# Performance work log

Measured on AMD Instinct MI355X. Metric: run time of the kernel, lower is better.

The kernel has to match this reference:

```python
import jax, jax.numpy as jnp
import numpy as np

E = 8      # n_rm_states
D = 256    # flattened input dim
H = 64     # hidden width (hard-coded in module)
A = 18     # n_actions
B = 65536  # batch


def setup_inputs() -> dict:
    key = jax.random.key(0)
    ks = jax.random.split(key, 16)
    s = lambda k, shape, fan_in: jax.random.normal(k, shape, jnp.float32) * (1.0 / np.sqrt(fan_in))
    inp = {
        "state": jax.random.normal(ks[0], (B, D), jnp.float32),
        "rm_state": jax.random.randint(ks[1], (B,), 0, E),
        # stacked per-expert params: layer i weight [E, in, out], bias [E, out]
        "W1": s(ks[2], (E, D, H), D), "b1": jnp.zeros((E, H), jnp.float32),
        "W2": s(ks[3], (E, H, H), H), "b2": jnp.zeros((E, H), jnp.float32),
        "W3": s(ks[4], (E, H, H), H), "b3": jnp.zeros((E, H), jnp.float32),
        "W4": s(ks[5], (E, H, H), H), "b4": jnp.zeros((E, H), jnp.float32),
        "W5": s(ks[6], (E, H, H), H), "b5": jnp.zeros((E, H), jnp.float32),
        "W6": s(ks[7], (E, H, A), H), "b6": jnp.zeros((E, A), jnp.float32),
    }
    return inp


def reference(state, rm_state, W1, b1, W2, b2, W3, b3, W4, b4, W5, b5, W6, b6):
    x = state.reshape(state.shape[0], -1)              # [B, D]
    # Run all E expert MLPs densely over the batch, then select per-row expert.
    h = jax.nn.relu(jnp.einsum('bd,edh->ebh', x, W1) + b1[:, None, :])   # [E, B, H]
    h = jax.nn.relu(jnp.einsum('ebh,ehk->ebk', h, W2) + b2[:, None, :])
    h = jax.nn.relu(jnp.einsum('ebh,ehk->ebk', h, W3) + b3[:, None, :])
    h = jax.nn.relu(jnp.einsum('ebh,ehk->ebk', h, W4) + b4[:, None, :])
    h = jax.nn.relu(jnp.einsum('ebh,ehk->ebk', h, W5) + b5[:, None, :])
    out_all = jnp.einsum('ebh,eha->eba', h, W6) + b6[:, None, :]          # [E, B, A]
    # scatter-back: actions[b] = expert[rm_state[b]](x[b])
    actions = out_all[rm_state, jnp.arange(x.shape[0])]                    # [B, A]
    return actions
```

## Files before the change

kernel.cpp:

```cpp
#include <hip/hip_runtime.h>
#include <hip/hip_bf16.h>


#define NE   8
#define DIM  256
#define HID  64
#define NA   18

typedef __attribute__((ext_vector_type(8))) short short8;
typedef __attribute__((ext_vector_type(4))) float f32x4;
#define MFMA __builtin_amdgcn_mfma_f32_16x16x32_bf16

__device__ __forceinline__ unsigned short f2bf(float f) {
    unsigned u = __builtin_bit_cast(unsigned, f);
    u += 0x7fff + ((u >> 16) & 1);
    return (unsigned short)(u >> 16);
}
__device__ __forceinline__ float bf2f(unsigned short h) {
    unsigned u = ((unsigned)h) << 16;
    return __builtin_bit_cast(float, u);
}
__device__ __forceinline__ void split8v(const float* xs, short8& hi, short8& lo) {
    float back[8];
    #pragma unroll
    for (int p = 0; p < 4; ++p) {
        __hip_bfloat162 h2 = __float22bfloat162_rn(make_float2(xs[2*p], xs[2*p+1]));
        hi[2*p]   = (short)__builtin_bit_cast(unsigned short, h2.x);
        hi[2*p+1] = (short)__builtin_bit_cast(unsigned short, h2.y);
        float2 b2 = __bfloat1622float2(h2);
        back[2*p] = b2.x; back[2*p+1] = b2.y;
    }
    #pragma unroll
    for (int p = 0; p < 4; ++p) {
        __hip_bfloat162 l2 = __float22bfloat162_rn(
            make_float2(xs[2*p] - back[2*p], xs[2*p+1] - back[2*p+1]));
        lo[2*p]   = (short)__builtin_bit_cast(unsigned short, l2.x);
        lo[2*p+1] = (short)__builtin_bit_cast(unsigned short, l2.y);
    }
}

__global__ __launch_bounds__(256) void prep_histo(
    const float* __restrict__ W1, const float* __restrict__ W2,
    const float* __restrict__ W3, const float* __restrict__ W4,
    const float* __restrict__ W5, const float* __restrict__ W6,
    short* __restrict__ W1H, short* __restrict__ W1L,
    short* __restrict__ W2H, short* __restrict__ W2L,
    short* __restrict__ W3H, short* __restrict__ W3L,
    short* __restrict__ W4H, short* __restrict__ W4L,
    short* __restrict__ W5H, short* __restrict__ W5L,
    short* __restrict__ W6H, short* __restrict__ W6L,
    const int* __restrict__ rm, int* __restrict__ hist) {
    const int bid = blockIdx.x;
    if (bid >= 136) {
        __shared__ int wch[4][NE];
        const int blk = bid - 136;
        const int t = threadIdx.x, w = t >> 6, l = t & 63;
        const int e = rm[blk * 256 + t];
        #pragma unroll
        for (int q = 0; q < NE; ++q) {
            unsigned long long m = __ballot(e == q);
            if (l == 0) wch[w][q] = __popcll(m);
        }
        __syncthreads();
        if (t < NE) hist[blk * NE + t] = wch[0][t] + wch[1][t] + wch[2][t] + wch[3][t];
        return;
    }
    const int u = bid * 256 + threadIdx.x;
    const float* src; int sstride, dbase, n, npad;
    short *H, *L;
    if (u < 16384) {
        int e = u >> 11, r = u & 2047;
        int ks = r >> 8, nt = (r >> 6) & 3, l = r & 63;
        int k0 = ks * 32 + ((l >> 4) << 3); n = (nt << 4) + (l & 15);
        src = W1 + ((size_t)(e * DIM + k0)) * HID + n;
        sstride = HID; npad = HID;
        H = W1H; L = W1L; dbase = e * 16384 + ((ks * 4 + nt) * 64 + l) * 8;
    } else if (u < 32768) {
        int u2 = u - 16384;
        int layer = u2 >> 12, local = u2 & 4095;
        int e = local >> 9, r = local & 511;
        int ks = r >> 8, nt = (r >> 6) & 3, l = r & 63;
        int k0 = ks * 32 + ((l >> 4) << 3); n = (nt << 4) + (l & 15);
        const float* W = (layer == 0) ? W2 : (layer == 1) ? W3 : (layer == 2) ? W4 : W5;
        src = W + ((size_t)(e * HID + k0)) * HID + n;
        sstride = HID; npad = HID;
        H = (layer == 0) ? W2H : (layer == 1) ? W3H : (layer == 2) ? W4H : W5H;
        L = (layer == 0) ? W2L : (layer == 1) ? W3L : (layer == 2) ? W4L : W5L;
        dbase = e * 4096 + ((ks * 4 + nt) * 64 + l) * 8;
    } else {
        int u3 = u - 32768;
        int e = u3 >> 8, r = u3 & 255;
        int ks = r >> 7, nt = (r >> 6) & 1, l = r & 63;
        int k0 = ks * 32 + ((l >> 4) << 3); n = (nt << 4) + (l & 15);
        src = W6 + ((size_t)(e * HID + k0)) * NA + n;
        sstride = NA; npad = NA;
        H = W6H; L = W6L; dbase = e * 2048 + ((ks * 2 + nt) * 64 + l) * 8;
    }
    short8 hs, ls;
    #pragma unroll
    for (int j = 0; j < 8; ++j) {
        float v = (n < npad) ? src[j * sstride] : 0.0f;
        unsigned short h = f2bf(v);
        hs[j] = (short)h;
        ls[j] = (short)f2bf(v - bf2f(h));
    }
    *(short8*)(H + dbase) = hs;
    *(short8*)(L + dbase) = ls;
}

__global__ __launch_bounds__(512) void scan_scatter(const int* __restrict__ rm,
                                                    const int* __restrict__ hist,
                                                    int* __restrict__ perm,
                                                    int* __restrict__ meta) {
    __shared__ int sbuf[NE][256];
    __shared__ int wc[8][NE];
    __shared__ int wb2[4][NE];
    __shared__ int baseE[NE];
    const int t = threadIdx.x, w = t >> 6, l = t & 63;
    const int myblk = blockIdx.x;

    {
        int v0 = hist[(l * 4 + 0) * NE + w];
        int v1 = hist[(l * 4 + 1) * NE + w];
        int v2 = hist[(l * 4 + 2) * NE + w];
        int v3 = hist[(l * 4 + 3) * NE + w];
        v1 += v0; v2 += v1; v3 += v2;
        int s = v3;
        #pragma unroll
        for (int off = 1; off < 64; off <<= 1) {
            int u = __shfl_up(s, off);
            if (l >= off) s += u;
        }
        const int ex = s - v3;
        sbuf[w][l * 4 + 0] = ex + v0;
        sbuf[w][l * 4 + 1] = ex + v1;
        sbuf[w][l * 4 + 2] = ex + v2;
        sbuf[w][l * 4 + 3] = ex + v3;
    }
    __syncthreads();
    if (t < NE) {
        int es = 0;
        for (int q = 0; q < t; ++q) es += sbuf[q][255];
        baseE[t] = es + (myblk ? sbuf[t][myblk - 1] : 0);
    }
    if (myblk == 0 && t == 0) {
        int es = 0, ts = 0;
        meta[8] = 0; meta[17] = 0;
        for (int e = 0; e < NE; ++e) {
            int c = sbuf[e][255];
            meta[e] = c;
            es += c; meta[8 + e + 1] = es;
            ts += (c + 31) >> 5; meta[17 + e + 1] = ts;
        }
    }
    const int i = myblk * 256 + t;
    const int e_row = (t < 256) ? rm[i] : -1;
    const unsigned long long ltm = (1ull << l) - 1ull;
    int rank = 0;
    #pragma unroll
    for (int q = 0; q < NE; ++q) {
        unsigned long long m = __ballot(e_row == q);
        if (e_row == q) rank = __popcll(m & ltm);
        if (l == 0) wc[w][q] = __popcll(m);
    }
    __syncthreads();
    if (t < 32) {
        int ww = t >> 3, q = t & 7;
        int b = baseE[q];
        for (int p = 0; p < ww; ++p) b += wc[p][q];
        wb2[ww][q] = b;
    }
    __syncthreads();
    if (t < 256) perm[wb2[w][e_row] + rank] = i;
}

__device__ __forceinline__ void read_split(const float* pa, const float* pb, int off,
                                           short8& hi, short8& lo) {
    float4 a0 = *(const float4*)(pa + off);
    float4 a1 = *(const float4*)(pa + off + 4);
    float4 b0 = *(const float4*)(pb + off);
    float4 b1 = *(const float4*)(pb + off + 4);
    float xs[8] = {fmaxf(a0.x + b0.x, 0.0f), fmaxf(a0.y + b0.y, 0.0f),
                   fmaxf(a0.z + b0.z, 0.0f), fmaxf(a0.w + b0.w, 0.0f),
                   fmaxf(a1.x + b1.x, 0.0f), fmaxf(a1.y + b1.y, 0.0f),
                   fmaxf(a1.z + b1.z, 0.0f), fmaxf(a1.w + b1.w, 0.0f)};
    split8v(xs, hi, lo);
}

template <int NT>
__device__ __forceinline__ void mfma_slice(const short* __restrict__ WH,
                                           const short* __restrict__ WL,
                                           int l, int kh,
                                           const short8& ahi, const short8& alo,
                                           f32x4* acc) {
    #pragma unroll
    for (int nt = 0; nt < NT; ++nt) {
        short8 bh = *(const short8*)(WH + (kh * NT + nt) * 512 + l * 8);
        short8 bl = *(const short8*)(WL + (kh * NT + nt) * 512 + l * 8);
        acc[nt] = MFMA(ahi, bh, acc[nt], 0, 0, 0);
        acc[nt] = MFMA(alo, bh, acc[nt], 0, 0, 0);
        acc[nt] = MFMA(ahi, bl, acc[nt], 0, 0, 0);
    }
}

template <int NT>
__device__ __forceinline__ void write_partial(float* pw, int l,
                                              const float* __restrict__ bias,
                                              const f32x4* acc) {
    const int lg = l >> 4, lr = l & 15;
    #pragma unroll
    for (int nt = 0; nt < NT; ++nt) {
        float bv = bias ? bias[nt * 16 + lr] : 0.0f;
        #pragma unroll
        for (int r = 0; r < 4; ++r)
            pw[(lg * 4 + r) * 68 + nt * 16 + lr] = acc[nt][r] + bv;
    }
}

__global__ __launch_bounds__(256, 8) void mlp_mfma(
    const float* __restrict__ x, const int* __restrict__ perm,
    const int* __restrict__ meta,
    const short* __restrict__ W1H, const short* __restrict__ W1L,
    const short* __restrict__ W2H, const short* __restrict__ W2L,
    const short* __restrict__ W3H, const short* __restrict__ W3L,
    const short* __restrict__ W4H, const short* __restrict__ W4L,
    const short* __restrict__ W5H, const short* __restrict__ W5L,
    const short* __restrict__ W6H, const short* __restrict__ W6L,
    const float* __restrict__ b1, const float* __restrict__ b2,
    const float* __restrict__ b3, const float* __restrict__ b4,
    const float* __restrict__ b5, const float* __restrict__ b6,
    float* __restrict__ out) {
    __shared__ __align__(16) float hbuf[2][2][16][68];
    const int blk = blockIdx.x;
    if (blk >= meta[17 + NE]) return;
    int e = 0;
    #pragma unroll 1
    while (blk >= meta[17 + e + 1]) ++e;
    const int lt = blk - meta[17 + e];
    const int cnt = meta[e];
    const int pbase = meta[8 + e];
    const int t = threadIdx.x, w = t >> 6, l = t & 63;
    const int m = w >> 1, kh = w & 1;
    const int lg = l >> 4, lr = l & 15;
    const int li = lt * 32 + m * 16 + lr;
    const int row = perm[pbase + min(li, cnt - 1)];

    float* pw = &hbuf[kh][m][0][0];
    const float* pa = &hbuf[0][m][0][0];
    const float* pb = &hbuf[1][m][0][0];
    const int roff = lr * 68 + kh * 32 + lg * 8;
    const f32x4 zero = {0.0f, 0.0f, 0.0f, 0.0f};

    {
        f32x4 a0[4] = {zero, zero, zero, zero};
        f32x4 a1[4] = {zero, zero, zero, zero};
        const float* xr = x + (size_t)row * DIM + kh * 128 + lg * 8;
        const short* WHp = W1H + (size_t)e * 16384;
        const short* WLp = W1L + (size_t)e * 16384;
        #pragma unroll
        for (int ks = 0; ks < 4; ++ks) {
            float4 u0 = *(const float4*)(xr + ks * 32);
            float4 u1 = *(const float4*)(xr + ks * 32 + 4);
            float xs[8] = {u0.x, u0.y, u0.z, u0.w, u1.x, u1.y, u1.z, u1.w};
            short8 ahi, alo; split8v(xs, ahi, alo);
            const int ksg = kh * 4 + ks;
            #pragma unroll
            for (int nt = 0; nt < 4; ++nt) {
                short8 bh = *(const short8*)(WHp + (ksg * 4 + nt) * 512 + l * 8);
                short8 bl = *(const short8*)(WLp + (ksg * 4 + nt) * 512 + l * 8);
                a0[nt] = MFMA(ahi, bh, a0[nt], 0, 0, 0);
                a1[nt] = MFMA(alo, bh, a1[nt], 0, 0, 0);
                a1[nt] = MFMA(ahi, bl, a1[nt], 0, 0, 0);
            }
        }
        f32x4 acc[4];
        #pragma unroll
        for (int nt = 0; nt < 4; ++nt) acc[nt] = a0[nt] + a1[nt];
        write_partial<4>(pw, l, (kh == 0) ? b1 + e * HID : nullptr, acc);
    }
    __syncthreads();

    #define HIDDEN(WH_, WL_, bias_)                                          \
    {                                                                        \
        short8 ahi, alo;                                                     \
        read_split(pa, pb, roff, ahi, alo);                                  \
        __syncthreads();                    \
        f32x4 acc[4] = {zero, zero, zero, zero};                             \
        mfma_slice<4>(WH_ + e * 4096, WL_ + e * 4096, l, kh, ahi, alo, acc); \
        write_partial<4>(pw, l, (kh == 0) ? bias_ + e * HID : nullptr, acc); \
        __syncthreads();                   \
    }
    HIDDEN(W2H, W2L, b2)
    HIDDEN(W3H, W3L, b3)
    HIDDEN(W4H, W4L, b4)
    HIDDEN(W5H, W5L, b5)
    #undef HIDDEN

    {
        short8 ahi, alo;
        read_split(pa, pb, roff, ahi, alo);
        __syncthreads();
        f32x4 acc[2] = {zero, zero};
        mfma_slice<2>(W6H + e * 2048, W6L + e * 2048, l, kh, ahi, alo, acc);
        write_partial<2>(pw, l, nullptr, acc);
        __syncthreads();
    }
    const float* b6p = b6 + e * NA;
    #pragma unroll
    for (int idx = t; idx < 2 * 16 * NA; idx += 256) {
        const int m2 = idx / (16 * NA);
        const int rr = (idx % (16 * NA)) / NA;
        const int c  = idx % NA;
        const int gr = lt * 32 + m2 * 16 + rr;
        if (gr < cnt) {
            const int rowid = perm[pbase + gr];
            out[(size_t)rowid * NA + c] =
                hbuf[0][m2][rr][c] + hbuf[1][m2][rr][c] + b6p[c];
        }
    }
}

extern "C" void kernel_launch(void* const* d_in, const int* in_sizes, int n_in,
                              void* d_out, int out_size, void* d_ws, size_t ws_size,
                              hipStream_t stream) {
    const float* x  = (const float*)d_in[0];
    const int*   rm = (const int*)d_in[1];
    const float* W1 = (const float*)d_in[2];   const float* b1 = (const float*)d_in[3];
    const float* W2 = (const float*)d_in[4];   const float* b2 = (const float*)d_in[5];
    const float* W3 = (const float*)d_in[6];   const float* b3 = (const float*)d_in[7];
    const float* W4 = (const float*)d_in[8];   const float* b4 = (const float*)d_in[9];
    const float* W5 = (const float*)d_in[10];  const float* b5 = (const float*)d_in[11];
    const float* W6 = (const float*)d_in[12];  const float* b6 = (const float*)d_in[13];
    float* out = (float*)d_out;

    const int B = in_sizes[1];
    const int nblk = B / 256;

    int* hist = (int*)d_ws;
    int* meta = hist + nblk * NE;
    int* perm = meta + 32;
    short* W1H = (short*)(perm + B);
    short* W1L = W1H + 131072;
    short* W2H = W1L + 131072;  short* W2L = W2H + 32768;
    short* W3H = W2L + 32768;   short* W3L = W3H + 32768;
    short* W4H = W3L + 32768;   short* W4L = W4H + 32768;
    short* W5H = W4L + 32768;   short* W5L = W5H + 32768;
    short* W6H = W5L + 32768;   short* W6L = W6H + 16384;

    prep_histo<<<136 + nblk, 256, 0, stream>>>(W1, W2, W3, W4, W5, W6,
                                               W1H, W1L, W2H, W2L, W3H, W3L,
                                               W4H, W4L, W5H, W5L, W6H, W6L,
                                               rm, hist);
    scan_scatter<<<nblk, 512, 0, stream>>>(rm, hist, perm, meta);
    mlp_mfma<<<B / 32 + NE, 256, 0, stream>>>(x, perm, meta,
                                              W1H, W1L, W2H, W2L, W3H, W3L,
                                              W4H, W4L, W5H, W5L, W6H, W6L,
                                              b1, b2, b3, b4, b5, b6, out);
}
```

Measured before the change: 153.1 us.

## Switch MLP to 32x32x16 MFMA with 128-row tiles and weight prefetch

Replaces the 16x16x32 bf16 MFMA path with 32x32x16 MFMAs, repacking all weight fragments in the prep kernel to match the new operand layout. Each block now processes 128 rows with 512 threads instead of 32 rows with 256, so there are fewer tiles per expert, and the scan metadata is updated to count 128-row tiles. Weight fragments for the next layer are loaded into registers before the current layer's MFMAs to hide load latency. The trade-offs are higher register pressure, fewer resident blocks, and more padded work for experts whose row count is not a multiple of 128.

New measurement: 162.7 us. 6.2% more time.

```diff
diff --git a/kernel.cpp b/kernel.cpp
--- a/kernel.cpp
+++ b/kernel.cpp
@@ -7,9 +7,9 @@
 #define HID  64
 #define NA   18
 
-typedef __attribute__((ext_vector_type(8))) short short8;
-typedef __attribute__((ext_vector_type(4))) float f32x4;
-#define MFMA __builtin_amdgcn_mfma_f32_16x16x32_bf16
+typedef __attribute__((ext_vector_type(8)))  short short8;
+typedef __attribute__((ext_vector_type(16))) float f32x16;
+#define MFMA32 __builtin_amdgcn_mfma_f32_32x32x16_bf16
 
 __device__ __forceinline__ unsigned short f2bf(float f) {
     unsigned u = __builtin_bit_cast(unsigned, f);
@@ -70,31 +70,31 @@
     short *H, *L;
     if (u < 16384) {
         int e = u >> 11, r = u & 2047;
-        int ks = r >> 8, nt = (r >> 6) & 3, l = r & 63;
-        int k0 = ks * 32 + ((l >> 4) << 3); n = (nt << 4) + (l & 15);
+        int ks = r >> 7, nt = (r >> 6) & 1, l = r & 63;
+        int k0 = ks * 16 + ((l >> 5) << 3); n = (nt << 5) + (l & 31);
         src = W1 + ((size_t)(e * DIM + k0)) * HID + n;
         sstride = HID; npad = HID;
-        H = W1H; L = W1L; dbase = e * 16384 + ((ks * 4 + nt) * 64 + l) * 8;
+        H = W1H; L = W1L; dbase = e * 16384 + ((ks * 2 + nt) * 64 + l) * 8;
     } else if (u < 32768) {
         int u2 = u - 16384;
         int layer = u2 >> 12, local = u2 & 4095;
         int e = local >> 9, r = local & 511;
-        int ks = r >> 8, nt = (r >> 6) & 3, l = r & 63;
-        int k0 = ks * 32 + ((l >> 4) << 3); n = (nt << 4) + (l & 15);
+        int ks = r >> 7, nt = (r >> 6) & 1, l = r & 63;
+        int k0 = ks * 16 + ((l >> 5) << 3); n = (nt << 5) + (l & 31);
         const float* W = (layer == 0) ? W2 : (layer == 1) ? W3 : (layer == 2) ? W4 : W5;
         src = W + ((size_t)(e * HID + k0)) * HID + n;
         sstride = HID; npad = HID;
         H = (layer == 0) ? W2H : (layer == 1) ? W3H : (layer == 2) ? W4H : W5H;
         L = (layer == 0) ? W2L : (layer == 1) ? W3L : (layer == 2) ? W4L : W5L;
-        dbase = e * 4096 + ((ks * 4 + nt) * 64 + l) * 8;
+        dbase = e * 4096 + ((ks * 2 + nt) * 64 + l) * 8;
     } else {
         int u3 = u - 32768;
         int e = u3 >> 8, r = u3 & 255;
-        int ks = r >> 7, nt = (r >> 6) & 1, l = r & 63;
-        int k0 = ks * 32 + ((l >> 4) << 3); n = (nt << 4) + (l & 15);
+        int ks = r >> 6, l = r & 63;
+        int k0 = ks * 16 + ((l >> 5) << 3); n = l & 31;
         src = W6 + ((size_t)(e * HID + k0)) * NA + n;
         sstride = NA; npad = NA;
-        H = W6H; L = W6L; dbase = e * 2048 + ((ks * 2 + nt) * 64 + l) * 8;
+        H = W6H; L = W6L; dbase = e * 2048 + (ks * 64 + l) * 8;
     }
     short8 hs, ls;
     #pragma unroll
@@ -150,7 +150,7 @@
             int c = sbuf[e][255];
             meta[e] = c;
             es += c; meta[8 + e + 1] = es;
-            ts += (c + 31) >> 5; meta[17 + e + 1] = ts;
+            ts += (c + 127) >> 7; meta[17 + e + 1] = ts;
         }
     }
     const int i = myblk * 256 + t;
@@ -174,8 +174,8 @@
     if (t < 256) perm[wb2[w][e_row] + rank] = i;
 }
 
-__device__ __forceinline__ void read_split(const float* pa, const float* pb, int off,
-                                           short8& hi, short8& lo) {
+__device__ __forceinline__ void rs(const float* pa, const float* pb, int off,
+                                   short8& hi, short8& lo) {
     float4 a0 = *(const float4*)(pa + off);
     float4 a1 = *(const float4*)(pa + off + 4);
     float4 b0 = *(const float4*)(pb + off);
@@ -187,37 +187,64 @@
     split8v(xs, hi, lo);
 }
 
-template <int NT>
-__device__ __forceinline__ void mfma_slice(const short* __restrict__ WH,
-                                           const short* __restrict__ WL,
-                                           int l, int kh,
-                                           const short8& ahi, const short8& alo,
-                                           f32x4* acc) {
-    #pragma unroll
-    for (int nt = 0; nt < NT; ++nt) {
-        short8 bh = *(const short8*)(WH + (kh * NT + nt) * 512 + l * 8);
-        short8 bl = *(const short8*)(WL + (kh * NT + nt) * 512 + l * 8);
-        acc[nt] = MFMA(ahi, bh, acc[nt], 0, 0, 0);
-        acc[nt] = MFMA(alo, bh, acc[nt], 0, 0, 0);
-        acc[nt] = MFMA(ahi, bl, acc[nt], 0, 0, 0);
-    }
-}
-
-template <int NT>
-__device__ __forceinline__ void write_partial(float* pw, int l,
-                                              const float* __restrict__ bias,
-                                              const f32x4* acc) {
-    const int lg = l >> 4, lr = l & 15;
-    #pragma unroll
-    for (int nt = 0; nt < NT; ++nt) {
-        float bv = bias ? bias[nt * 16 + lr] : 0.0f;
+__device__ __forceinline__ void write16(float* pw, int lc, int lh,
+                                        const float* bias,
+                                        const f32x16& c0, const f32x16& c1) {
+    #pragma unroll
+    for (int nt = 0; nt < 2; ++nt) {
+        const f32x16& c = nt ? c1 : c0;
+        float bv = bias ? bias[nt * 32 + lc] : 0.0f;
         #pragma unroll
-        for (int r = 0; r < 4; ++r)
-            pw[(lg * 4 + r) * 68 + nt * 16 + lr] = acc[nt][r] + bv;
-    }
-}
-
-__global__ __launch_bounds__(256, 8) void mlp_mfma(
+        for (int r = 0; r < 16; ++r) {
+            int rw = (r & 3) + 8 * (r >> 2) + 4 * lh;
+            pw[rw * 66 + nt * 32 + lc] = c[r] + bv;
+        }
+    }
+}
+__device__ __forceinline__ void write16_1(float* pw, int lc, int lh,
+                                          const f32x16& c0) {
+    #pragma unroll
+    for (int r = 0; r < 16; ++r) {
+        int rw = (r & 3) + 8 * (r >> 2) + 4 * lh;
+        pw[rw * 66 + lc] = c0[r];
+    }
+}
+
+#define PF4(nm, ph, pl)                                    \
+    nm##h0 = *(const short8*)(ph);                         \
+    nm##h1 = *(const short8*)((ph) + 512);                 \
+    nm##h2 = *(const short8*)((ph) + 1024);                \
+    nm##h3 = *(const short8*)((ph) + 1536);                \
+    nm##l0 = *(const short8*)(pl);                         \
+    nm##l1 = *(const short8*)((pl) + 512);                 \
+    nm##l2 = *(const short8*)((pl) + 1024);                \
+    nm##l3 = *(const short8*)((pl) + 1536);
+
+#define HIDDEN(nm, PREFETCH, biasp)                                           \
+    {                                                                         \
+        short8 a0h, a0l, a1h, a1l;                                            \
+        rs(pa, pb, roff, a0h, a0l);                                           \
+        rs(pa, pb, roff + 16, a1h, a1l);                                      \
+        PREFETCH                                                              \
+        __syncthreads();                                                      \
+        f32x16 c0 = {}, c1 = {};                                              \
+        c0 = MFMA32(a0h, nm##h0, c0, 0, 0, 0);                                \
+        c0 = MFMA32(a0l, nm##h0, c0, 0, 0, 0);                                \
+        c0 = MFMA32(a0h, nm##l0, c0, 0, 0, 0);                                \
+        c1 = MFMA32(a0h, nm##h1, c1, 0, 0, 0);                                \
+        c1 = MFMA32(a0l, nm##h1, c1, 0, 0, 0);                                \
+        c1 = MFMA32(a0h, nm##l1, c1, 0, 0, 0);                                \
+        c0 = MFMA32(a1h, nm##h2, c0, 0, 0, 0);                                \
+        c0 = MFMA32(a1l, nm##h2, c0, 0, 0, 0);                                \
+        c0 = MFMA32(a1h, nm##l2, c0, 0, 0, 0);                                \
+        c1 = MFMA32(a1h, nm##h3, c1, 0, 0, 0);                                \
+        c1 = MFMA32(a1l, nm##h3, c1, 0, 0, 0);                                \
+        c1 = MFMA32(a1h, nm##l3, c1, 0, 0, 0);                                \
+        write16(pw, lc, lh, biasp, c0, c1);                                   \
+        __syncthreads();                                                      \
+    }
+
+__global__ __launch_bounds__(512, 4) void mlp_mfma(
     const float* __restrict__ x, const int* __restrict__ perm,
     const int* __restrict__ meta,
     const short* __restrict__ W1H, const short* __restrict__ W1L,
@@ -230,7 +257,7 @@
     const float* __restrict__ b3, const float* __restrict__ b4,
     const float* __restrict__ b5, const float* __restrict__ b6,
     float* __restrict__ out) {
-    __shared__ __align__(16) float hbuf[2][2][16][68];
+    __shared__ __align__(16) float hbuf[2][4][32][66];
     const int blk = blockIdx.x;
     if (blk >= meta[17 + NE]) return;
     int e = 0;
@@ -241,77 +268,91 @@
     const int pbase = meta[8 + e];
     const int t = threadIdx.x, w = t >> 6, l = t & 63;
     const int m = w >> 1, kh = w & 1;
-    const int lg = l >> 4, lr = l & 15;
-    const int li = lt * 32 + m * 16 + lr;
+    const int lc = l & 31, lh = l >> 5;
+    const int li = lt * 128 + m * 32 + lc;
     const int row = perm[pbase + min(li, cnt - 1)];
 
     float* pw = &hbuf[kh][m][0][0];
     const float* pa = &hbuf[0][m][0][0];
     const float* pb = &hbuf[1][m][0][0];
-    const int roff = lr * 68 + kh * 32 + lg * 8;
-    const f32x4 zero = {0.0f, 0.0f, 0.0f, 0.0f};
+    const int roff = lc * 66 + kh * 32 + lh * 8;
+
+    const short* pW1h = W1H + e * 16384 + kh * 8192 + l * 8;
+    const short* pW1l = W1L + e * 16384 + kh * 8192 + l * 8;
+    const short* pW2h = W2H + e * 4096 + kh * 2048 + l * 8;
+    const short* pW2l = W2L + e * 4096 + kh * 2048 + l * 8;
+    const short* pW3h = W3H + e * 4096 + kh * 2048 + l * 8;
+    const short* pW3l = W3L + e * 4096 + kh * 2048 + l * 8;
+    const short* pW4h = W4H + e * 4096 + kh * 2048 + l * 8;
+    const short* pW4l = W4L + e * 4096 + kh * 2048 + l * 8;
+    const short* pW5h = W5H + e * 4096 + kh * 2048 + l * 8;
+    const short* pW5l = W5L + e * 4096 + kh * 2048 + l * 8;
+    const short* pW6h = W6H + e * 2048 + kh * 1024 + l * 8;
+    const short* pW6l = W6L + e * 2048 + kh * 1024 + l * 8;
+
+    short8 f2h0, f2h1, f2h2, f2h3, f2l0, f2l1, f2l2, f2l3;
+    short8 f3h0, f3h1, f3h2, f3h3, f3l0, f3l1, f3l2, f3l3;
+    short8 f4h0, f4h1, f4h2, f4h3, f4l0, f4l1, f4l2, f4l3;
+    short8 f5h0, f5h1, f5h2, f5h3, f5l0, f5l1, f5l2, f5l3;
+    short8 f6h0, f6h1, f6l0, f6l1;
 
     {
-        f32x4 a0[4] = {zero, zero, zero, zero};
-        f32x4 a1[4] = {zero, zero, zero, zero};
-        const float* xr = x + (size_t)row * DIM + kh * 128 + lg * 8;
-        const short* WHp = W1H + (size_t)e * 16384;
-        const short* WLp = W1L + (size_t)e * 16384;
+        f32x16 c0 = {}, c1 = {};
+        const float* xr = x + (size_t)row * DIM + kh * 128 + lh * 8;
         #pragma unroll
-        for (int ks = 0; ks < 4; ++ks) {
-            float4 u0 = *(const float4*)(xr + ks * 32);
-            float4 u1 = *(const float4*)(xr + ks * 32 + 4);
+        for (int ks = 0; ks < 8; ++ks) {
+            float4 u0 = *(const float4*)(xr + ks * 16);
+            float4 u1 = *(const float4*)(xr + ks * 16 + 4);
             float xs[8] = {u0.x, u0.y, u0.z, u0.w, u1.x, u1.y, u1.z, u1.w};
-            short8 ahi, alo; split8v(xs, ahi, alo);
-            const int ksg = kh * 4 + ks;
-            #pragma unroll
-            for (int nt = 0; nt < 4; ++nt) {
-                short8 bh = *(const short8*)(WHp + (ksg * 4 + nt) * 512 + l * 8);
-                short8 bl = *(const short8*)(WLp + (ksg * 4 + nt) * 512 + l * 8);
-                a0[nt] = MFMA(ahi, bh, a0[nt], 0, 0, 0);
-                a1[nt] = MFMA(alo, bh, a1[nt], 0, 0, 0);
-                a1[nt] = MFMA(ahi, bl, a1[nt], 0, 0, 0);
-            }
-        }
-        f32x4 acc[4];
-        #pragma unroll
-        for (int nt = 0; nt < 4; ++nt) acc[nt] = a0[nt] + a1[nt];
-        write_partial<4>(pw, l, (kh == 0) ? b1 + e * HID : nullptr, acc);
-    }
-    __syncthreads();
-
-    #define HIDDEN(WH_, WL_, bias_)                                          \
-    {                                                                        \
-        short8 ahi, alo;                                                     \
-        read_split(pa, pb, roff, ahi, alo);                                  \
-        __syncthreads();                    \
-        f32x4 acc[4] = {zero, zero, zero, zero};                             \
-        mfma_slice<4>(WH_ + e * 4096, WL_ + e * 4096, l, kh, ahi, alo, acc); \
-        write_partial<4>(pw, l, (kh == 0) ? bias_ + e * HID : nullptr, acc); \
-        __syncthreads();                   \
-    }
-    HIDDEN(W2H, W2L, b2)
-    HIDDEN(W3H, W3L, b3)
-    HIDDEN(W4H, W4L, b4)
-    HIDDEN(W5H, W5L, b5)
-    #undef HIDDEN
+            short8 ah, al; split8v(xs, ah, al);
+            short8 bh0 = *(const short8*)(pW1h + (ks * 2 + 0) * 512);
+            short8 bl0 = *(const short8*)(pW1l + (ks * 2 + 0) * 512);
+            short8 bh1 = *(const short8*)(pW1h + (ks * 2 + 1) * 512);
+            short8 bl1 = *(const short8*)(pW1l + (ks * 2 + 1) * 512);
+            c0 = MFMA32(ah, bh0, c0, 0, 0, 0);
+            c0 = MFMA32(al, bh0, c0, 0, 0, 0);
+            c0 = MFMA32(ah, bl0, c0, 0, 0, 0);
+            c1 = MFMA32(ah, bh1, c1, 0, 0, 0);
+            c1 = MFMA32(al, bh1, c1, 0, 0, 0);
+            c1 = MFMA32(ah, bl1, c1, 0, 0, 0);
+        }
+        PF4(f2, pW2h, pW2l)
+        write16(pw, lc, lh, (kh == 0) ? b1 + e * HID : nullptr, c0, c1);
+        __syncthreads();
+    }
+
+    HIDDEN(f2, PF4(f3, pW3h, pW3l), (kh == 0) ? b2 + e * HID : nullptr)
+    HIDDEN(f3, PF4(f4, pW4h, pW4l), (kh == 0) ? b3 + e * HID : nullptr)
+    HIDDEN(f4, PF4(f5, pW5h, pW5l), (kh == 0) ? b4 + e * HID : nullptr)
+    HIDDEN(f5,
+           f6h0 = *(const short8*)(pW6h);
+           f6h1 = *(const short8*)(pW6h + 512);
+           f6l0 = *(const short8*)(pW6l);
+           f6l1 = *(const short8*)(pW6l + 512);,
+           (kh == 0) ? b5 + e * HID : nullptr)
 
     {
-        short8 ahi, alo;
-        read_split(pa, pb, roff, ahi, alo);
+        short8 a0h, a0l, a1h, a1l;
+        rs(pa, pb, roff, a0h, a0l);
+        rs(pa, pb, roff + 16, a1h, a1l);
         __syncthreads();
-        f32x4 acc[2] = {zero, zero};
-        mfma_slice<2>(W6H + e * 2048, W6L + e * 2048, l, kh, ahi, alo, acc);
-        write_partial<2>(pw, l, nullptr, acc);
+        f32x16 c0 = {};
+        c0 = MFMA32(a0h, f6h0, c0, 0, 0, 0);
+        c0 = MFMA32(a0l, f6h0, c0, 0, 0, 0);
+        c0 = MFMA32(a0h, f6l0, c0, 0, 0, 0);
+        c0 = MFMA32(a1h, f6h1, c0, 0, 0, 0);
+        c0 = MFMA32(a1l, f6h1, c0, 0, 0, 0);
+        c0 = MFMA32(a1h, f6l1, c0, 0, 0, 0);
+        write16_1(pw, lc, lh, c0);
         __syncthreads();
     }
+
     const float* b6p = b6 + e * NA;
-    #pragma unroll
-    for (int idx = t; idx < 2 * 16 * NA; idx += 256) {
-        const int m2 = idx / (16 * NA);
-        const int rr = (idx % (16 * NA)) / NA;
+    for (int idx = t; idx < 4 * 32 * NA; idx += 512) {
+        const int m2 = idx / (32 * NA);
+        const int rr = (idx / NA) % 32;
         const int c  = idx % NA;
-        const int gr = lt * 32 + m2 * 16 + rr;
+        const int gr = lt * 128 + m2 * 32 + rr;
         if (gr < cnt) {
             const int rowid = perm[pbase + gr];
             out[(size_t)rowid * NA + c] =
@@ -352,8 +393,8 @@
                                                W4H, W4L, W5H, W5L, W6H, W6L,
                                                rm, hist);
     scan_scatter<<<nblk, 512, 0, stream>>>(rm, hist, perm, meta);
-    mlp_mfma<<<B / 32 + NE, 256, 0, stream>>>(x, perm, meta,
-                                              W1H, W1L, W2H, W2L, W3H, W3L,
-                                              W4H, W4L, W5H, W5L, W6H, W6L,
-                                              b1, b2, b3, b4, b5, b6, out);
-}
+    mlp_mfma<<<B / 128 + NE, 512, 0, stream>>>(x, perm, meta,
+                                               W1H, W1L, W2H, W2L, W3H, W3L,
+                                               W4H, W4L, W5H, W5L, W6H, W6L,
+                                               b1, b2, b3, b4, b5, b6, out);
+}
```

## Switch MLP to 32x32 MFMA with 128-row tiles and LDS-staged weights

Applied to the files above, without the earlier changes.

Reworks the grouped MLP kernel to use 32x32x16 bf16 MFMA instructions, with each wave owning 32 rows, so a block now handles 128 rows instead of 32. Weight fragments are double-buffered through LDS, with each step's global load overlapped with the previous step's compute, and the prep kernel's fragment layout and tile counts are changed to match. This removes the cross-wave K-split partial sums and their extra LDS reduction, and amortises weight loads over more rows. In exchange it raises LDS and register use (launch bounds drop from 8 to 3 blocks per SM) and wastes more padded rows for small experts.

Result: no change. 153.4 us (+0.2%).

```diff
diff --git a/kernel.cpp b/kernel.cpp
--- a/kernel.cpp
+++ b/kernel.cpp
@@ -7,9 +7,9 @@
 #define HID  64
 #define NA   18
 
-typedef __attribute__((ext_vector_type(8))) short short8;
-typedef __attribute__((ext_vector_type(4))) float f32x4;
-#define MFMA __builtin_amdgcn_mfma_f32_16x16x32_bf16
+typedef __attribute__((ext_vector_type(8)))  short short8;
+typedef __attribute__((ext_vector_type(16))) float f32x16;
+#define MFMA32 __builtin_amdgcn_mfma_f32_32x32x16_bf16
 
 __device__ __forceinline__ unsigned short f2bf(float f) {
     unsigned u = __builtin_bit_cast(unsigned, f);
@@ -70,31 +70,31 @@
     short *H, *L;
     if (u < 16384) {
         int e = u >> 11, r = u & 2047;
-        int ks = r >> 8, nt = (r >> 6) & 3, l = r & 63;
-        int k0 = ks * 32 + ((l >> 4) << 3); n = (nt << 4) + (l & 15);
+        int ks = r >> 7, nt = (r >> 6) & 1, l = r & 63;
+        int k0 = ks * 16 + ((l >> 5) << 3); n = (nt << 5) + (l & 31);
         src = W1 + ((size_t)(e * DIM + k0)) * HID + n;
         sstride = HID; npad = HID;
-        H = W1H; L = W1L; dbase = e * 16384 + ((ks * 4 + nt) * 64 + l) * 8;
+        H = W1H; L = W1L; dbase = e * 16384 + ((ks * 2 + nt) * 64 + l) * 8;
     } else if (u < 32768) {
         int u2 = u - 16384;
         int layer = u2 >> 12, local = u2 & 4095;
         int e = local >> 9, r = local & 511;
-        int ks = r >> 8, nt = (r >> 6) & 3, l = r & 63;
-        int k0 = ks * 32 + ((l >> 4) << 3); n = (nt << 4) + (l & 15);
+        int ks = r >> 7, nt = (r >> 6) & 1, l = r & 63;
+        int k0 = ks * 16 + ((l >> 5) << 3); n = (nt << 5) + (l & 31);
         const float* W = (layer == 0) ? W2 : (layer == 1) ? W3 : (layer == 2) ? W4 : W5;
         src = W + ((size_t)(e * HID + k0)) * HID + n;
         sstride = HID; npad = HID;
         H = (layer == 0) ? W2H : (layer == 1) ? W3H : (layer == 2) ? W4H : W5H;
         L = (layer == 0) ? W2L : (layer == 1) ? W3L : (layer == 2) ? W4L : W5L;
-        dbase = e * 4096 + ((ks * 4 + nt) * 64 + l) * 8;
+        dbase = e * 4096 + ((ks * 2 + nt) * 64 + l) * 8;
     } else {
         int u3 = u - 32768;
         int e = u3 >> 8, r = u3 & 255;
-        int ks = r >> 7, nt = (r >> 6) & 1, l = r & 63;
-        int k0 = ks * 32 + ((l >> 4) << 3); n = (nt << 4) + (l & 15);
+        int ks = r >> 6, l = r & 63;
+        int k0 = ks * 16 + ((l >> 5) << 3); n = l & 31;
         src = W6 + ((size_t)(e * HID + k0)) * NA + n;
         sstride = NA; npad = NA;
-        H = W6H; L = W6L; dbase = e * 2048 + ((ks * 2 + nt) * 64 + l) * 8;
+        H = W6H; L = W6L; dbase = e * 2048 + (ks * 64 + l) * 8;
     }
     short8 hs, ls;
     #pragma unroll
@@ -150,7 +150,7 @@
             int c = sbuf[e][255];
             meta[e] = c;
             es += c; meta[8 + e + 1] = es;
-            ts += (c + 31) >> 5; meta[17 + e + 1] = ts;
+            ts += (c + 127) >> 7; meta[17 + e + 1] = ts;
         }
     }
     const int i = myblk * 256 + t;
@@ -174,50 +174,7 @@
     if (t < 256) perm[wb2[w][e_row] + rank] = i;
 }
 
-__device__ __forceinline__ void read_split(const float* pa, const float* pb, int off,
-                                           short8& hi, short8& lo) {
-    float4 a0 = *(const float4*)(pa + off);
-    float4 a1 = *(const float4*)(pa + off + 4);
-    float4 b0 = *(const float4*)(pb + off);
-    float4 b1 = *(const float4*)(pb + off + 4);
-    float xs[8] = {fmaxf(a0.x + b0.x, 0.0f), fmaxf(a0.y + b0.y, 0.0f),
-                   fmaxf(a0.z + b0.z, 0.0f), fmaxf(a0.w + b0.w, 0.0f),
-                   fmaxf(a1.x + b1.x, 0.0f), fmaxf(a1.y + b1.y, 0.0f),
-                   fmaxf(a1.z + b1.z, 0.0f), fmaxf(a1.w + b1.w, 0.0f)};
-    split8v(xs, hi, lo);
-}
-
-template <int NT>
-__device__ __forceinline__ void mfma_slice(const short* __restrict__ WH,
-                                           const short* __restrict__ WL,
-                                           int l, int kh,
-                                           const short8& ahi, const short8& alo,
-                                           f32x4* acc) {
-    #pragma unroll
-    for (int nt = 0; nt < NT; ++nt) {
-        short8 bh = *(const short8*)(WH + (kh * NT + nt) * 512 + l * 8);
-        short8 bl = *(const short8*)(WL + (kh * NT + nt) * 512 + l * 8);
-        acc[nt] = MFMA(ahi, bh, acc[nt], 0, 0, 0);
-        acc[nt] = MFMA(alo, bh, acc[nt], 0, 0, 0);
-        acc[nt] = MFMA(ahi, bl, acc[nt], 0, 0, 0);
-    }
-}
-
-template <int NT>
-__device__ __forceinline__ void write_partial(float* pw, int l,
-                                              const float* __restrict__ bias,
-                                              const f32x4* acc) {
-    const int lg = l >> 4, lr = l & 15;
-    #pragma unroll
-    for (int nt = 0; nt < NT; ++nt) {
-        float bv = bias ? bias[nt * 16 + lr] : 0.0f;
-        #pragma unroll
-        for (int r = 0; r < 4; ++r)
-            pw[(lg * 4 + r) * 68 + nt * 16 + lr] = acc[nt][r] + bv;
-    }
-}
-
-__global__ __launch_bounds__(256, 8) void mlp_mfma(
+__global__ __launch_bounds__(256, 3) void mlp_mfma(
     const float* __restrict__ x, const int* __restrict__ perm,
     const int* __restrict__ meta,
     const short* __restrict__ W1H, const short* __restrict__ W1L,
@@ -230,7 +187,8 @@
     const float* __restrict__ b3, const float* __restrict__ b4,
     const float* __restrict__ b5, const float* __restrict__ b6,
     float* __restrict__ out) {
-    __shared__ __align__(16) float hbuf[2][2][16][68];
+    __shared__ __align__(16) float hbuf[4][32][66];
+    __shared__ __align__(16) short frag[2][4096];
     const int blk = blockIdx.x;
     if (blk >= meta[17 + NE]) return;
     int e = 0;
@@ -240,84 +198,135 @@
     const int cnt = meta[e];
     const int pbase = meta[8 + e];
     const int t = threadIdx.x, w = t >> 6, l = t & 63;
-    const int m = w >> 1, kh = w & 1;
-    const int lg = l >> 4, lr = l & 15;
-    const int li = lt * 32 + m * 16 + lr;
+    const int lc = l & 31, lh = l >> 5;
+    const int li = lt * 128 + w * 32 + lc;
     const int row = perm[pbase + min(li, cnt - 1)];
-
-    float* pw = &hbuf[kh][m][0][0];
-    const float* pa = &hbuf[0][m][0][0];
-    const float* pb = &hbuf[1][m][0][0];
-    const int roff = lr * 68 + kh * 32 + lg * 8;
-    const f32x4 zero = {0.0f, 0.0f, 0.0f, 0.0f};
-
+    float* hw = &hbuf[w][0][0];
+
+#define SRC_H(s) ((s) < 8 ? W1H + e * 16384 + (s) * 2048 :                    \
+                  (s) < 10 ? W2H + e * 4096 + ((s) & 1) * 2048 :              \
+                  (s) < 12 ? W3H + e * 4096 + ((s) & 1) * 2048 :              \
+                  (s) < 14 ? W4H + e * 4096 + ((s) & 1) * 2048 :              \
+                  (s) < 16 ? W5H + e * 4096 + ((s) & 1) * 2048 :              \
+                             W6H + e * 2048)
+#define SRC_L(s) ((s) < 8 ? W1L + e * 16384 + (s) * 2048 :                    \
+                  (s) < 10 ? W2L + e * 4096 + ((s) & 1) * 2048 :              \
+                  (s) < 12 ? W3L + e * 4096 + ((s) & 1) * 2048 :              \
+                  (s) < 14 ? W4L + e * 4096 + ((s) & 1) * 2048 :              \
+                  (s) < 16 ? W5L + e * 4096 + ((s) & 1) * 2048 :              \
+                             W6L + e * 2048)
+
+    short8 g0, g1;
+#define LOADG(s) { g0 = *(const short8*)(SRC_H(s) + t * 8);                   \
+                   g1 = *(const short8*)(SRC_L(s) + t * 8); }
+#define PUTG(b)  { *(short8*)(&frag[b][t * 8]) = g0;                          \
+                   *(short8*)(&frag[b][2048 + t * 8]) = g1; }
+
+#define MF3(AH, AL, BH, BL, C)                                                \
+    C = MFMA32(AH, BH, C, 0, 0, 0);                                           \
+    C = MFMA32(AL, BH, C, 0, 0, 0);                                           \
+    C = MFMA32(AH, BL, C, 0, 0, 0);
+
+    f32x16 c0 = {}, c1 = {};
+    const f32x16 fz = {};
+
+#define W1STEP(b, s) {                                                        \
+    const float* xr = x + (size_t)row * DIM + (s) * 32 + lh * 8;              \
+    _Pragma("unroll") for (int kk = 0; kk < 2; ++kk) {                        \
+        float4 u0 = *(const float4*)(xr + kk * 16);                           \
+        float4 u1 = *(const float4*)(xr + kk * 16 + 4);                       \
+        float xs[8] = {u0.x, u0.y, u0.z, u0.w, u1.x, u1.y, u1.z, u1.w};       \
+        short8 ah, al; split8v(xs, ah, al);                                   \
+        short8 bh0 = *(const short8*)(&frag[b][(kk * 2 + 0) * 512 + l * 8]);  \
+        short8 bl0 = *(const short8*)(&frag[b][2048 + (kk * 2 + 0) * 512 + l * 8]); \
+        short8 bh1 = *(const short8*)(&frag[b][(kk * 2 + 1) * 512 + l * 8]);  \
+        short8 bl1 = *(const short8*)(&frag[b][2048 + (kk * 2 + 1) * 512 + l * 8]); \
+        MF3(ah, al, bh0, bl0, c0)                                             \
+        MF3(ah, al, bh1, bl1, c1)                                             \
+    } }
+
+#define HSTEP(b, hf) {                                                        \
+    _Pragma("unroll") for (int kk = 0; kk < 2; ++kk) {                        \
+        const float* ap = hw + lc * 66 + ((hf) * 2 + kk) * 16 + lh * 8;       \
+        float4 u0 = *(const float4*)(ap);                                     \
+        float4 u1 = *(const float4*)(ap + 4);                                 \
+        float xs[8] = {u0.x, u0.y, u0.z, u0.w, u1.x, u1.y, u1.z, u1.w};       \
+        short8 ah, al; split8v(xs, ah, al);                                   \
+        short8 bh0 = *(const short8*)(&frag[b][(kk * 2 + 0) * 512 + l * 8]);  \
+        short8 bl0 = *(const short8*)(&frag[b][2048 + (kk * 2 + 0) * 512 + l * 8]); \
+        short8 bh1 = *(const short8*)(&frag[b][(kk * 2 + 1) * 512 + l * 8]);  \
+        short8 bl1 = *(const short8*)(&frag[b][2048 + (kk * 2 + 1) * 512 + l * 8]); \
+        MF3(ah, al, bh0, bl0, c0)                                             \
+        MF3(ah, al, bh1, bl1, c1)                                             \
+    } }
+
+#define WRITE16(biasp) {                                                      \
+    const float* bp = (biasp);                                                \
+    _Pragma("unroll") for (int nt = 0; nt < 2; ++nt) {                        \
+        const f32x16& c = nt ? c1 : c0;                                       \
+        float bv = bp[nt * 32 + lc];                                          \
+        _Pragma("unroll") for (int r = 0; r < 16; ++r) {                      \
+            int rw = (r & 3) + 8 * (r >> 2) + 4 * lh;                         \
+            hw[rw * 66 + nt * 32 + lc] = fmaxf(c[r] + bv, 0.0f);              \
+        } } }
+
+    LOADG(0); PUTG(0); LOADG(1);
+    __syncthreads();
+    W1STEP(0, 0)
+    PUTG(1); LOADG(2);  __syncthreads(); W1STEP(1, 1)
+    PUTG(0); LOADG(3);  __syncthreads(); W1STEP(0, 2)
+    PUTG(1); LOADG(4);  __syncthreads(); W1STEP(1, 3)
+    PUTG(0); LOADG(5);  __syncthreads(); W1STEP(0, 4)
+    PUTG(1); LOADG(6);  __syncthreads(); W1STEP(1, 5)
+    PUTG(0); LOADG(7);  __syncthreads(); W1STEP(0, 6)
+    PUTG(1); LOADG(8);  __syncthreads(); W1STEP(1, 7)
+    WRITE16(b1 + e * HID); c0 = fz; c1 = fz;
+    PUTG(0); LOADG(9);  __syncthreads(); HSTEP(0, 0)
+    PUTG(1); LOADG(10); __syncthreads(); HSTEP(1, 1)
+    WRITE16(b2 + e * HID); c0 = fz; c1 = fz;
+    PUTG(0); LOADG(11); __syncthreads(); HSTEP(0, 0)
+    PUTG(1); LOADG(12); __syncthreads(); HSTEP(1, 1)
+    WRITE16(b3 + e * HID); c0 = fz; c1 = fz;
+    PUTG(0); LOADG(13); __syncthreads(); HSTEP(0, 0)
+    PUTG(1); LOADG(14); __syncthreads(); HSTEP(1, 1)
+    WRITE16(b4 + e * HID); c0 = fz; c1 = fz;
+    PUTG(0); LOADG(15); __syncthreads(); HSTEP(0, 0)
+    PUTG(1); LOADG(16); __syncthreads(); HSTEP(1, 1)
+    WRITE16(b5 + e * HID); c0 = fz; c1 = fz;
+    PUTG(0); __syncthreads();
     {
-        f32x4 a0[4] = {zero, zero, zero, zero};
-        f32x4 a1[4] = {zero, zero, zero, zero};
-        const float* xr = x + (size_t)row * DIM + kh * 128 + lg * 8;
-        const short* WHp = W1H + (size_t)e * 16384;
-        const short* WLp = W1L + (size_t)e * 16384;
         #pragma unroll
-        for (int ks = 0; ks < 4; ++ks) {
-            float4 u0 = *(const float4*)(xr + ks * 32);
-            float4 u1 = *(const float4*)(xr + ks * 32 + 4);
+        for (int kk = 0; kk < 4; ++kk) {
+            const float* ap = hw + lc * 66 + kk * 16 + lh * 8;
+            float4 u0 = *(const float4*)(ap);
+            float4 u1 = *(const float4*)(ap + 4);
             float xs[8] = {u0.x, u0.y, u0.z, u0.w, u1.x, u1.y, u1.z, u1.w};
-            short8 ahi, alo; split8v(xs, ahi, alo);
-            const int ksg = kh * 4 + ks;
-            #pragma unroll
-            for (int nt = 0; nt < 4; ++nt) {
-                short8 bh = *(const short8*)(WHp + (ksg * 4 + nt) * 512 + l * 8);
-                short8 bl = *(const short8*)(WLp + (ksg * 4 + nt) * 512 + l * 8);
-                a0[nt] = MFMA(ahi, bh, a0[nt], 0, 0, 0);
-                a1[nt] = MFMA(alo, bh, a1[nt], 0, 0, 0);
-                a1[nt] = MFMA(ahi, bl, a1[nt], 0, 0, 0);
-            }
+            short8 ah, al; split8v(xs, ah, al);
+            short8 bh = *(const short8*)(&frag[0][kk * 512 + l * 8]);
+            short8 bl = *(const short8*)(&frag[0][2048 + kk * 512 + l * 8]);
+            MF3(ah, al, bh, bl, c0)
         }
-        f32x4 acc[4];
-        #pragma unroll
-        for (int nt = 0; nt < 4; ++nt) acc[nt] = a0[nt] + a1[nt];
-        write_partial<4>(pw, l, (kh == 0) ? b1 + e * HID : nullptr, acc);
-    }
-    __syncthreads();
-
-    #define HIDDEN(WH_, WL_, bias_)                                          \
-    {                                                                        \
-        short8 ahi, alo;                                                     \
-        read_split(pa, pb, roff, ahi, alo);                                  \
-        __syncthreads();                    \
-        f32x4 acc[4] = {zero, zero, zero, zero};                             \
-        mfma_slice<4>(WH_ + e * 4096, WL_ + e * 4096, l, kh, ahi, alo, acc); \
-        write_partial<4>(pw, l, (kh == 0) ? bias_ + e * HID : nullptr, acc); \
-        __syncthreads();                   \
-    }
-    HIDDEN(W2H, W2L, b2)
-    HIDDEN(W3H, W3L, b3)
-    HIDDEN(W4H, W4L, b4)
-    HIDDEN(W5H, W5L, b5)
-    #undef HIDDEN
-
-    {
-        short8 ahi, alo;
-        read_split(pa, pb, roff, ahi, alo);
-        __syncthreads();
-        f32x4 acc[2] = {zero, zero};
-        mfma_slice<2>(W6H + e * 2048, W6L + e * 2048, l, kh, ahi, alo, acc);
-        write_partial<2>(pw, l, nullptr, acc);
-        __syncthreads();
+    }
+    #pragma unroll
+    for (int r = 0; r < 16; ++r) {
+        int rw = (r & 3) + 8 * (r >> 2) + 4 * lh;
+        hw[rw * 66 + lc] = c0[r];
     }
     const float* b6p = b6 + e * NA;
-    #pragma unroll
-    for (int idx = t; idx < 2 * 16 * NA; idx += 256) {
-        const int m2 = idx / (16 * NA);
-        const int rr = (idx % (16 * NA)) / NA;
-        const int c  = idx % NA;
-        const int gr = lt * 32 + m2 * 16 + rr;
-        if (gr < cnt) {
-            const int rowid = perm[pbase + gr];
-            out[(size_t)rowid * NA + c] =
-                hbuf[0][m2][rr][c] + hbuf[1][m2][rr][c] + b6p[c];
-        }
-    }
+    for (int i = l; i < 32 * NA; i += 64) {
+        int rr = i / NA, cc = i % NA;
+        int gr = lt * 128 + w * 32 + rr;
+        if (gr < cnt)
+            out[(size_t)perm[pbase + gr] * NA + cc] = hw[rr * 66 + cc] + b6p[cc];
+    }
+#undef SRC_H
+#undef SRC_L
+#undef LOADG
+#undef PUTG
+#undef MF3
+#undef W1STEP
+#undef HSTEP
+#undef WRITE16
 }
 
 extern "C" void kernel_launch(void* const* d_in, const int* in_sizes, int n_in,
@@ -352,8 +361,8 @@
                                                W4H, W4L, W5H, W5L, W6H, W6L,
                                                rm, hist);
     scan_scatter<<<nblk, 512, 0, stream>>>(rm, hist, perm, meta);
-    mlp_mfma<<<B / 32 + NE, 256, 0, stream>>>(x, perm, meta,
-                                              W1H, W1L, W2H, W2L, W3H, W3L,
-                                              W4H, W4L, W5H, W5L, W6H, W6L,
-                                              b1, b2, b3, b4, b5, b6, out);
-}
+    mlp_mfma<<<B / 128 + NE, 256, 0, stream>>>(x, perm, meta,
+                                               W1H, W1L, W2H, W2L, W3H, W3L,
+                                               W4H, W4L, W5H, W5L, W6H, W6L,
+                                               b1, b2, b3, b4, b5, b6, out);
+}
```
